# Performance work log

Measured on AMD Instinct MI355X. Metric: run time of the kernel, lower is better.

Reference implementation:

```python
import jax, jax.numpy as jnp
import numpy as np

DIM = 384
HEADS = 12
HD = DIM // HEADS  # 32
WIN = 16
N = WIN * WIN      # 256
B = 256            # num_windows * batch
K = 5              # dwc kernel size
EPS = 1e-6


def setup_inputs() -> dict:
    key = jax.random.key(0)
    ks = jax.random.split(key, 8)
    u = lambda k, shape, fan_in: jax.random.uniform(
        k, shape, jnp.float32, -1.0 / np.sqrt(fan_in), 1.0 / np.sqrt(fan_in))
    return {
        "x": jax.random.normal(ks[0], (B, N, DIM), jnp.float32),
        # nn.Linear(dim, 3*dim): weight [3C, C], bias [3C]
        "qkv_w": u(ks[1], (3 * DIM, DIM), DIM),
        "qkv_b": u(ks[2], (3 * DIM,), DIM),
        # nn.Parameter initialized to zeros
        "pos_enc": jnp.zeros((1, N, DIM), jnp.float32),
        # depthwise Conv2d(HD, HD, K, groups=HD): weight [HD, 1, K, K]
        "dwc_w": u(ks[3], (HD, 1, K, K), K * K),
        "dwc_b": u(ks[4], (HD,), K * K),
        "proj_w": u(ks[5], (DIM, DIM), DIM),
        "proj_b": u(ks[6], (DIM,), DIM),
    }


def reference(x, qkv_w, qkv_b, pos_enc, dwc_w, dwc_b, proj_w, proj_b):
    Bsz, Nn, C = x.shape
    qkv = x @ qkv_w.T + qkv_b                     # [B, N, 3C]
    q, k, v = jnp.split(qkv, 3, axis=-1)          # each [B, N, C]
    k = k + pos_enc
    q = jax.nn.relu(q)
    k = jax.nn.relu(k)

    def to_heads(t):  # 'b n (h c) -> (b h) n c'
        return t.reshape(Bsz, Nn, HEADS, HD).transpose(0, 2, 1, 3).reshape(Bsz * HEADS, Nn, HD)

    q, k, v = to_heads(q), to_heads(k), to_heads(v)
    # explicit fp32 (autocast disabled block in original)
    qf = q.astype(jnp.float32)
    kf = k.astype(jnp.float32)
    vf = v.astype(jnp.float32)

    z = 1.0 / (jnp.einsum('bic,bc->bi', qf, kf.sum(axis=1)) + EPS)  # [BH, N]

    i = j = Nn
    c = d = HD
    if i * j * (c + d) > c * d * (i + j):  # kv-first (true for N=256, HD=32)
        kv = jnp.einsum('bjc,bjd->bcd', kf, vf)            # [BH, c, d]
        out = jnp.einsum('bic,bcd,bi->bid', qf, kv, z)     # [BH, N, d]
    else:
        qk = jnp.einsum('bic,bjc->bij', qf, kf)
        out = jnp.einsum('bij,bjd,bi->bid', qk, vf, z)

    # depthwise conv on v: 'b (w h) c -> b c w h'
    num = int(Nn ** 0.5)
    fm = vf.reshape(Bsz * HEADS, num, num, HD).transpose(0, 3, 1, 2)  # NCHW
    fm = jax.lax.conv_general_dilated(
        fm, dwc_w, window_strides=(1, 1),
        padding=[(K // 2, K // 2), (K // 2, K // 2)],
        dimension_numbers=('NCHW', 'OIHW', 'NCHW'),
        feature_group_count=HD)
    fm = fm + dwc_b[None, :, None, None]
    fm = fm.transpose(0, 2, 3, 1).reshape(Bsz * HEADS, Nn, HD)  # 'b c w h -> b (w h) c'

    out = out + fm
    # '(b h) n c -> b n (h c)'
    out = out.reshape(Bsz, HEADS, Nn, HD).transpose(0, 2, 1, 3).reshape(Bsz, Nn, C)
    return out @ proj_w.T + proj_b
```

## Files before the change

### kernel.cpp

```cpp
#include <hip/hip_runtime.h>
#include <stdint.h>
#include <stddef.h>


typedef _Float16 f16;
typedef __attribute__((ext_vector_type(4))) _Float16 f16x4;
typedef __attribute__((ext_vector_type(8))) _Float16 f16x8;
typedef __attribute__((ext_vector_type(4))) float floatx4;

#define DEV __device__ __forceinline__

DEV void async16(const void* g, void* l) {
  __builtin_amdgcn_global_load_lds(
      (const __attribute__((address_space(1))) void*)g,
      (__attribute__((address_space(3))) void*)l,
      16, 0, 0);
}

DEV floatx4 mfma16(f16x8 a, f16x8 b, floatx4 c) {
  return __builtin_amdgcn_mfma_f32_16x16x32_f16(a, b, c, 0, 0, 0);
}

DEV f16x4 cvt4(float4 v) {
  f16x4 h;
  h[0] = (f16)v.x; h[1] = (f16)v.y; h[2] = (f16)v.z; h[3] = (f16)v.w;
  return h;
}

__global__ __launch_bounds__(256) void qkv_kernel(
    const float* __restrict__ A, const float* __restrict__ W,
    const float* __restrict__ bias, const float* __restrict__ pos,
    f16* __restrict__ q_ws, f16* __restrict__ kT_ws, f16* __restrict__ vT_ws) {
  __shared__ __align__(16) f16 Af[128 * 40];
  __shared__ __align__(16) f16 Wf[128 * 40];
  const int tid = threadIdx.x;
  const int lane = tid & 63, wave = tid >> 6;
  const int quad = lane >> 4, lr = lane & 15;
  const int wm = wave >> 1, wn = wave & 1;
  const int bx = blockIdx.x;
  const int ga = bx / 72, rem = bx - ga * 72;
  const int nblk = rem >> 3, gc = rem & 7;
  const int m0 = (ga * 8 + gc) * 128, n0 = nblk * 128;
  const int srow = tid >> 3, sg = tid & 7;

  floatx4 acc[4][4] = {};
  float4 pa[4], pw[4];

#pragma unroll
  for (int rr = 0; rr < 4; ++rr) {
    const int row = rr * 32 + srow;
    pa[rr] = *(const float4*)(A + (size_t)(m0 + row) * 384 + sg * 4);
    pw[rr] = *(const float4*)(W + (size_t)(n0 + row) * 384 + sg * 4);
  }

  for (int kt = 0; kt < 12; ++kt) {
    __syncthreads();
#pragma unroll
    for (int rr = 0; rr < 4; ++rr) {
      const int row = rr * 32 + srow;
      *(f16x4*)(Af + row * 40 + sg * 4) = cvt4(pa[rr]);
      *(f16x4*)(Wf + row * 40 + sg * 4) = cvt4(pw[rr]);
    }
    __syncthreads();
    if (kt < 11) {
      const int k0 = (kt + 1) * 32;
#pragma unroll
      for (int rr = 0; rr < 4; ++rr) {
        const int row = rr * 32 + srow;
        pa[rr] = *(const float4*)(A + (size_t)(m0 + row) * 384 + k0 + sg * 4);
        pw[rr] = *(const float4*)(W + (size_t)(n0 + row) * 384 + k0 + sg * 4);
      }
    }
    f16x8 af[4], wf[4];
#pragma unroll
    for (int mt = 0; mt < 4; ++mt)
      af[mt] = *(const f16x8*)(Af + (wm * 64 + mt * 16 + lr) * 40 + quad * 8);
#pragma unroll
    for (int nt = 0; nt < 4; ++nt)
      wf[nt] = *(const f16x8*)(Wf + (wn * 64 + nt * 16 + lr) * 40 + quad * 8);
#pragma unroll
    for (int mt = 0; mt < 4; ++mt)
#pragma unroll
      for (int nt = 0; nt < 4; ++nt)
        acc[mt][nt] = mfma16(af[mt], wf[nt], acc[mt][nt]);
  }

  float bv[4];
#pragma unroll
  for (int nt = 0; nt < 4; ++nt)
    bv[nt] = bias[n0 + wn * 64 + nt * 16 + lr];

  const int cls = nblk / 3;
  const int cbase = (nblk - cls * 3) * 128;
  if (cls == 0) {
#pragma unroll
    for (int mt = 0; mt < 4; ++mt) {
#pragma unroll
      for (int r = 0; r < 4; ++r) {
        const int m = m0 + wm * 64 + mt * 16 + quad * 4 + r;
        const int bwin = m >> 8, t = m & 255;
#pragma unroll
        for (int nt = 0; nt < 4; ++nt) {
          const int c = cbase + wn * 64 + nt * 16 + lr;
          const int h = c >> 5, hd = c & 31;
          const float val = fmaxf(acc[mt][nt][r] + bv[nt], 0.f);
          q_ws[(size_t)(bwin * 12 + h) * 8192 + t * 32 + hd] = (f16)val;
        }
      }
    }
  } else {
#pragma unroll
    for (int mt = 0; mt < 4; ++mt) {
      const int mb = m0 + wm * 64 + mt * 16 + quad * 4;
      const int bwin = mb >> 8, t0 = mb & 255;
#pragma unroll
      for (int nt = 0; nt < 4; ++nt) {
        const int c = cbase + wn * 64 + nt * 16 + lr;
        const int h = c >> 5, hd = c & 31;
        f16x4 pk;
        if (cls == 1) {
#pragma unroll
          for (int r = 0; r < 4; ++r)
            pk[r] = (f16)fmaxf(acc[mt][nt][r] + bv[nt] + pos[(t0 + r) * 384 + c], 0.f);
          *(f16x4*)(kT_ws + (size_t)(bwin * 12 + h) * 8192 + hd * 256 + t0) = pk;
        } else {
#pragma unroll
          for (int r = 0; r < 4; ++r)
            pk[r] = (f16)(acc[mt][nt][r] + bv[nt]);
          *(f16x4*)(vT_ws + (size_t)(bwin * 12 + h) * 8192 + hd * 256 + t0) = pk;
        }
      }
    }
  }
}

__global__ __launch_bounds__(256) void attn_kernel(
    const f16* __restrict__ q_ws, const f16* __restrict__ kT_ws,
    const f16* __restrict__ vT_ws, const float* __restrict__ dwc_w,
    const float* __restrict__ dwc_b, f16* __restrict__ y_ws) {
  __shared__ __align__(16) char khb[16640];
  __shared__ __align__(16) char vhb[16640];
  __shared__ __align__(16) float pkv[4 * 32 * 36];
  __shared__ float psum[8 * 32];
  __shared__ float ksum[32];
  __shared__ float zbuf[256];
  __shared__ __align__(16) f16 kvT[32 * 40];

  const int tid = threadIdx.x;
  const int lane = tid & 63, wave = tid >> 6;
  const int quad = lane >> 4, lr = lane & 15;
  const int bh = blockIdx.x;
  const size_t base = (size_t)bh * 8192;

#pragma unroll
  for (int t2 = 0; t2 < 4; ++t2) {
    const int is = wave * 4 + t2;
    async16(kT_ws + base + is * 512 + lane * 8, khb + is * 1040);
    async16(vT_ws + base + is * 512 + lane * 8, vhb + is * 1040);
  }
  __syncthreads();

  {
    const int c = tid & 31, seg = tid >> 5;
    const char* kr = khb + (c >> 1) * 1040 + (c & 1) * 512;
    float s = 0.f;
#pragma unroll
    for (int j8 = 0; j8 < 32; j8 += 8) {
      f16x8 a = *(const f16x8*)(kr + (seg * 32 + j8) * 2);
#pragma unroll
      for (int j = 0; j < 8; ++j) s += (float)a[j];
    }
    psum[seg * 32 + c] = s;
  }
  {
    floatx4 kacc[2][2] = {};
#pragma unroll
    for (int ss = 0; ss < 2; ++ss) {
      const int s = wave * 2 + ss;
      f16x8 ka[2], vb[2];
#pragma unroll
      for (int m2 = 0; m2 < 2; ++m2) {
        const int c = m2 * 16 + lr;
        const size_t off =
            (size_t)(c >> 1) * 1040 + (c & 1) * 512 + (s * 32 + quad * 8) * 2;
        ka[m2] = *(const f16x8*)(khb + off);
        vb[m2] = *(const f16x8*)(vhb + off);
      }
#pragma unroll
      for (int m2 = 0; m2 < 2; ++m2)
#pragma unroll
        for (int n2 = 0; n2 < 2; ++n2)
          kacc[m2][n2] = mfma16(ka[m2], vb[n2], kacc[m2][n2]);
    }
#pragma unroll
    for (int m2 = 0; m2 < 2; ++m2)
#pragma unroll
      for (int n2 = 0; n2 < 2; ++n2)
#pragma unroll
        for (int r = 0; r < 4; ++r)
          pkv[(wave * 32 + m2 * 16 + quad * 4 + r) * 36 + n2 * 16 + lr] =
              kacc[m2][n2][r];
  }
  __syncthreads();

  if (tid < 32) {
    float s = 0.f;
#pragma unroll
    for (int seg = 0; seg < 8; ++seg) s += psum[seg * 32 + tid];
    ksum[tid] = s;
  }
  {
    const int c = tid >> 3, d0 = (tid & 7) * 4;
#pragma unroll
    for (int dd = 0; dd < 4; ++dd) {
      const int d = d0 + dd;
      float s = pkv[(0 * 32 + c) * 36 + d] + pkv[(1 * 32 + c) * 36 + d] +
                pkv[(2 * 32 + c) * 36 + d] + pkv[(3 * 32 + c) * 36 + d];
      kvT[d * 40 + c] = (f16)s;
    }
  }
  {
    uint32_t* fmu = (uint32_t*)khb;
    const int cg = tid & 15, xr = tid >> 4, c0 = cg * 2;
    float a0[16], a1[16];
    const float b0v = dwc_b[c0], b1v = dwc_b[c0 + 1];
#pragma unroll
    for (int yy = 0; yy < 16; ++yy) { a0[yy] = b0v; a1[yy] = b1v; }
    const char* v0 = vhb + cg * 1040;
#pragma unroll
    for (int dx = 0; dx < 5; ++dx) {
      const int xx = xr + dx - 2;
      if (xx < 0 || xx > 15) continue;
      float r0[16], r1[16];
      f16x8 h0 = *(const f16x8*)(v0 + xx * 32);
      f16x8 h1 = *(const f16x8*)(v0 + xx * 32 + 16);
      f16x8 h2 = *(const f16x8*)(v0 + 512 + xx * 32);
      f16x8 h3 = *(const f16x8*)(v0 + 512 + xx * 32 + 16);
#pragma unroll
      for (int j = 0; j < 8; ++j) {
        r0[j] = (float)h0[j]; r0[8 + j] = (float)h1[j];
        r1[j] = (float)h2[j]; r1[8 + j] = (float)h3[j];
      }
#pragma unroll
      for (int dy = 0; dy < 5; ++dy) {
        const float w0 = dwc_w[c0 * 25 + dx * 5 + dy];
        const float w1 = dwc_w[(c0 + 1) * 25 + dx * 5 + dy];
#pragma unroll
        for (int yy = 0; yy < 16; ++yy) {
          const int ys = yy + dy - 2;
          if (ys >= 0 && ys < 16) {
            a0[yy] += w0 * r0[ys];
            a1[yy] += w1 * r1[ys];
          }
        }
      }
    }
#pragma unroll
    for (int yy = 0; yy < 16; ++yy) {
      const uint32_t lo = (uint32_t)__builtin_bit_cast(uint16_t, (f16)a0[yy]);
      const uint32_t hi = (uint32_t)__builtin_bit_cast(uint16_t, (f16)a1[yy]);
      fmu[(xr * 16 + yy) * 16 + cg] = lo | (hi << 16);
    }
  }
  __syncthreads();

  {
    const f16* qrow = q_ws + base + (size_t)tid * 32;
    float dot = 0.f;
#pragma unroll
    for (int c8 = 0; c8 < 32; c8 += 8) {
      f16x8 qq = *(const f16x8*)(qrow + c8);
#pragma unroll
      for (int j = 0; j < 8; ++j) dot += (float)qq[j] * ksum[c8 + j];
    }
    zbuf[tid] = 1.f / (dot + 1e-6f);
  }
  {
    floatx4 oacc[4][2] = {};
    f16x8 qa[4], kb[2];
#pragma unroll
    for (int mm = 0; mm < 4; ++mm)
      qa[mm] = *(const f16x8*)(q_ws + base +
                               (size_t)(wave * 64 + mm * 16 + lr) * 32 + quad * 8);
#pragma unroll
    for (int nt = 0; nt < 2; ++nt)
      kb[nt] = *(const f16x8*)(kvT + (nt * 16 + lr) * 40 + quad * 8);
#pragma unroll
    for (int mm = 0; mm < 4; ++mm)
#pragma unroll
      for (int nt = 0; nt < 2; ++nt)
        oacc[mm][nt] = mfma16(qa[mm], kb[nt], oacc[mm][nt]);

    const f16* fmb = (const f16*)khb;
#pragma unroll
    for (int mm = 0; mm < 4; ++mm) {
#pragma unroll
      for (int r = 0; r < 4; ++r) {
        const int i = wave * 64 + mm * 16 + quad * 4 + r;
        const float zi = zbuf[i];
#pragma unroll
        for (int nt = 0; nt < 2; ++nt) {
          const int d = nt * 16 + lr;
          const float val = oacc[mm][nt][r] * zi + (float)fmb[i * 32 + d];
          y_ws[base + (size_t)i * 32 + d] = (f16)val;
        }
      }
    }
  }
}

__global__ __launch_bounds__(256) void proj_kernel(
    const f16* __restrict__ Y, const float* __restrict__ W,
    const float* __restrict__ bias, float* __restrict__ out) {
  __shared__ __align__(16) f16 Af[128 * 32];
  __shared__ __align__(16) f16 Wf[128 * 40];
  const int tid = threadIdx.x;
  const int lane = tid & 63, wave = tid >> 6;
  const int quad = lane >> 4, lr = lane & 15;
  const int wm = wave >> 1, wn = wave & 1;
  const int bx = blockIdx.x;
  const int ga = bx / 24, rem = bx - ga * 24;
  const int nblk = rem >> 3, gc = rem & 7;
  const int m0 = (ga * 8 + gc) * 128, n0 = nblk * 128;
  const int bwin = m0 >> 8, tbase = m0 & 255;
  const int srow = tid >> 3, sg = tid & 7;

  floatx4 acc[4][4] = {};
  float4 pw[4];
#pragma unroll
  for (int rr = 0; rr < 4; ++rr)
    pw[rr] = *(const float4*)(W + (size_t)(n0 + rr * 32 + srow) * 384 + sg * 4);

  for (int kt = 0; kt < 12; ++kt) {
    __syncthreads();
    {
      const size_t hbase = (size_t)(bwin * 12 + kt) * 8192;
#pragma unroll
      for (int t2 = 0; t2 < 2; ++t2) {
        const int ch = wave * 2 + t2;
        const int trow = tbase + ch * 16 + (lane >> 2);
        async16(Y + hbase + (size_t)trow * 32 + (lane & 3) * 8,
                (char*)Af + ch * 1024);
      }
    }
#pragma unroll
    for (int rr = 0; rr < 4; ++rr)
      *(f16x4*)(Wf + (rr * 32 + srow) * 40 + sg * 4) = cvt4(pw[rr]);
    __syncthreads();
    if (kt < 11) {
      const int k0 = (kt + 1) * 32;
#pragma unroll
      for (int rr = 0; rr < 4; ++rr)
        pw[rr] = *(const float4*)(W + (size_t)(n0 + rr * 32 + srow) * 384 +
                                  k0 + sg * 4);
    }
    f16x8 af[4], wf[4];
#pragma unroll
    for (int mt = 0; mt < 4; ++mt)
      af[mt] = *(const f16x8*)(Af + (wm * 64 + mt * 16 + lr) * 32 + quad * 8);
#pragma unroll
    for (int nt = 0; nt < 4; ++nt)
      wf[nt] = *(const f16x8*)(Wf + (wn * 64 + nt * 16 + lr) * 40 + quad * 8);
#pragma unroll
    for (int mt = 0; mt < 4; ++mt)
#pragma unroll
      for (int nt = 0; nt < 4; ++nt)
        acc[mt][nt] = mfma16(af[mt], wf[nt], acc[mt][nt]);
  }

  float bv[4];
#pragma unroll
  for (int nt = 0; nt < 4; ++nt)
    bv[nt] = bias[n0 + wn * 64 + nt * 16 + lr];
#pragma unroll
  for (int mt = 0; mt < 4; ++mt)
#pragma unroll
    for (int r = 0; r < 4; ++r) {
      const int m = m0 + wm * 64 + mt * 16 + quad * 4 + r;
#pragma unroll
      for (int nt = 0; nt < 4; ++nt) {
        const int n = n0 + wn * 64 + nt * 16 + lr;
        out[(size_t)m * 384 + n] = acc[mt][nt][r] + bv[nt];
      }
    }
}

extern "C" void kernel_launch(void* const* d_in, const int* in_sizes, int n_in,
                              void* d_out, int out_size, void* d_ws, size_t ws_size,
                              hipStream_t stream) {
  const float* x = (const float*)d_in[0];
  const float* qkv_w = (const float*)d_in[1];
  const float* qkv_b = (const float*)d_in[2];
  const float* pos = (const float*)d_in[3];
  const float* dwc_w = (const float*)d_in[4];
  const float* dwc_b = (const float*)d_in[5];
  const float* proj_w = (const float*)d_in[6];
  const float* proj_b = (const float*)d_in[7];
  float* out = (float*)d_out;

  const size_t WS_NEEDED = 150994944;
  if (ws_size < WS_NEEDED) return;

  char* ws = (char*)d_ws;
  f16* q_ws = (f16*)(ws);
  f16* kT_ws = (f16*)(ws + 50331648);
  f16* vT_ws = (f16*)(ws + 100663296);

  qkv_kernel<<<4608, 256, 0, stream>>>(x, qkv_w, qkv_b, pos,
                                       q_ws, kT_ws, vT_ws);
  attn_kernel<<<3072, 256, 0, stream>>>(q_ws, kT_ws, vT_ws,
                                        dwc_w, dwc_b, q_ws );
  proj_kernel<<<1536, 256, 0, stream>>>(q_ws, proj_w, proj_b, out);
}
```

Measured before the change: 408.4 us.

## Pre-convert GEMM operands to fp16 and stream tiles via async LDS loads

Adds a standalone fp32-to-fp16 conversion kernel for x, qkv_w and proj_w, storing the results in scratch space (the output buffer and the freed kT workspace region). The QKV and projection GEMMs then load fp16 tiles straight into XOR-swizzled shared memory with global_load_lds, using a K-tile of 64 instead of 32 and no register round trip or in-kernel conversion. This removes the per-tile conversion work and doubles the work per barrier. In exchange it adds an extra full read and write pass over x, and the async loads are no longer prefetched ahead of compute.

```diff
diff --git a/kernel.cpp b/kernel.cpp
--- a/kernel.cpp
+++ b/kernel.cpp
@@ -27,12 +27,21 @@
   return h;
 }
 
+__global__ __launch_bounds__(256) void cvt_kernel(
+    const float* __restrict__ src, f16* __restrict__ dst, int n4) {
+  const int stride = gridDim.x * 256;
+  for (int i = blockIdx.x * 256 + threadIdx.x; i < n4; i += stride) {
+    float4 v = ((const float4*)src)[i];
+    ((f16x4*)dst)[i] = cvt4(v);
+  }
+}
+
 __global__ __launch_bounds__(256) void qkv_kernel(
-    const float* __restrict__ A, const float* __restrict__ W,
+    const f16* __restrict__ A, const f16* __restrict__ W,
     const float* __restrict__ bias, const float* __restrict__ pos,
     f16* __restrict__ q_ws, f16* __restrict__ kT_ws, f16* __restrict__ vT_ws) {
-  __shared__ __align__(16) f16 Af[128 * 40];
-  __shared__ __align__(16) f16 Wf[128 * 40];
+  __shared__ __align__(16) f16 Af[128 * 64];
+  __shared__ __align__(16) f16 Wf[128 * 64];
   const int tid = threadIdx.x;
   const int lane = tid & 63, wave = tid >> 6;
   const int quad = lane >> 4, lr = lane & 15;
@@ -41,48 +50,47 @@
   const int ga = bx / 72, rem = bx - ga * 72;
   const int nblk = rem >> 3, gc = rem & 7;
   const int m0 = (ga * 8 + gc) * 128, n0 = nblk * 128;
-  const int srow = tid >> 3, sg = tid & 7;
+  const int rl = lane >> 3;
+  const int lcol = (lane & 7) ^ rl;
 
   floatx4 acc[4][4] = {};
-  float4 pa[4], pw[4];
-
-#pragma unroll
-  for (int rr = 0; rr < 4; ++rr) {
-    const int row = rr * 32 + srow;
-    pa[rr] = *(const float4*)(A + (size_t)(m0 + row) * 384 + sg * 4);
-    pw[rr] = *(const float4*)(W + (size_t)(n0 + row) * 384 + sg * 4);
-  }
-
-  for (int kt = 0; kt < 12; ++kt) {
+
+  const f16* ap[4];
+  const f16* wp[4];
+#pragma unroll
+  for (int t2 = 0; t2 < 4; ++t2) {
+    const int row = (wave * 4 + t2) * 8 + rl;
+    ap[t2] = A + (size_t)(m0 + row) * 384 + lcol * 8;
+    wp[t2] = W + (size_t)(n0 + row) * 384 + lcol * 8;
+  }
+
+  for (int kt = 0; kt < 6; ++kt) {
     __syncthreads();
 #pragma unroll
-    for (int rr = 0; rr < 4; ++rr) {
-      const int row = rr * 32 + srow;
-      *(f16x4*)(Af + row * 40 + sg * 4) = cvt4(pa[rr]);
-      *(f16x4*)(Wf + row * 40 + sg * 4) = cvt4(pw[rr]);
+    for (int t2 = 0; t2 < 4; ++t2) {
+      const int ch = wave * 4 + t2;
+      async16(ap[t2] + kt * 64, (char*)Af + ch * 1024);
+      async16(wp[t2] + kt * 64, (char*)Wf + ch * 1024);
     }
     __syncthreads();
-    if (kt < 11) {
-      const int k0 = (kt + 1) * 32;
-#pragma unroll
-      for (int rr = 0; rr < 4; ++rr) {
-        const int row = rr * 32 + srow;
-        pa[rr] = *(const float4*)(A + (size_t)(m0 + row) * 384 + k0 + sg * 4);
-        pw[rr] = *(const float4*)(W + (size_t)(n0 + row) * 384 + k0 + sg * 4);
-      }
-    }
-    f16x8 af[4], wf[4];
-#pragma unroll
-    for (int mt = 0; mt < 4; ++mt)
-      af[mt] = *(const f16x8*)(Af + (wm * 64 + mt * 16 + lr) * 40 + quad * 8);
-#pragma unroll
-    for (int nt = 0; nt < 4; ++nt)
-      wf[nt] = *(const f16x8*)(Wf + (wn * 64 + nt * 16 + lr) * 40 + quad * 8);
-#pragma unroll
-    for (int mt = 0; mt < 4; ++mt)
+#pragma unroll
+    for (int s = 0; s < 2; ++s) {
+      const int pc = ((quad + s * 4) ^ (lr & 7)) * 16;
+      f16x8 af[4], wf[4];
+#pragma unroll
+      for (int mt = 0; mt < 4; ++mt)
+        af[mt] = *(const f16x8*)((const char*)Af +
+                                 (wm * 64 + mt * 16 + lr) * 128 + pc);
 #pragma unroll
       for (int nt = 0; nt < 4; ++nt)
-        acc[mt][nt] = mfma16(af[mt], wf[nt], acc[mt][nt]);
+        wf[nt] = *(const f16x8*)((const char*)Wf +
+                                 (wn * 64 + nt * 16 + lr) * 128 + pc);
+#pragma unroll
+      for (int mt = 0; mt < 4; ++mt)
+#pragma unroll
+        for (int nt = 0; nt < 4; ++nt)
+          acc[mt][nt] = mfma16(af[mt], wf[nt], acc[mt][nt]);
+    }
   }
 
   float bv[4];
@@ -310,10 +318,10 @@
 }
 
 __global__ __launch_bounds__(256) void proj_kernel(
-    const f16* __restrict__ Y, const float* __restrict__ W,
+    const f16* __restrict__ Y, const f16* __restrict__ Wh,
     const float* __restrict__ bias, float* __restrict__ out) {
-  __shared__ __align__(16) f16 Af[128 * 32];
-  __shared__ __align__(16) f16 Wf[128 * 40];
+  __shared__ __align__(16) f16 Af[128 * 64];
+  __shared__ __align__(16) f16 Wf[128 * 64];
   const int tid = threadIdx.x;
   const int lane = tid & 63, wave = tid >> 6;
   const int quad = lane >> 4, lr = lane & 15;
@@ -323,49 +331,48 @@
   const int nblk = rem >> 3, gc = rem & 7;
   const int m0 = (ga * 8 + gc) * 128, n0 = nblk * 128;
   const int bwin = m0 >> 8, tbase = m0 & 255;
-  const int srow = tid >> 3, sg = tid & 7;
+  const int rl = lane >> 3;
+  const int lcol = (lane & 7) ^ rl;
 
   floatx4 acc[4][4] = {};
-  float4 pw[4];
-#pragma unroll
-  for (int rr = 0; rr < 4; ++rr)
-    pw[rr] = *(const float4*)(W + (size_t)(n0 + rr * 32 + srow) * 384 + sg * 4);
-
-  for (int kt = 0; kt < 12; ++kt) {
+
+  const f16* ap[4];
+  const f16* wp[4];
+#pragma unroll
+  for (int t2 = 0; t2 < 4; ++t2) {
+    const int rowl = (wave * 4 + t2) * 8 + rl;
+    ap[t2] = Y + (size_t)(bwin * 12 + (lcol >> 2)) * 8192 +
+             (size_t)(tbase + rowl) * 32 + (lcol & 3) * 8;
+    wp[t2] = Wh + (size_t)(n0 + rowl) * 384 + lcol * 8;
+  }
+
+  for (int kt = 0; kt < 6; ++kt) {
     __syncthreads();
-    {
-      const size_t hbase = (size_t)(bwin * 12 + kt) * 8192;
-#pragma unroll
-      for (int t2 = 0; t2 < 2; ++t2) {
-        const int ch = wave * 2 + t2;
-        const int trow = tbase + ch * 16 + (lane >> 2);
-        async16(Y + hbase + (size_t)trow * 32 + (lane & 3) * 8,
-                (char*)Af + ch * 1024);
-      }
-    }
-#pragma unroll
-    for (int rr = 0; rr < 4; ++rr)
-      *(f16x4*)(Wf + (rr * 32 + srow) * 40 + sg * 4) = cvt4(pw[rr]);
+#pragma unroll
+    for (int t2 = 0; t2 < 4; ++t2) {
+      const int ch = wave * 4 + t2;
+      async16(ap[t2] + (size_t)kt * 16384, (char*)Af + ch * 1024);
+      async16(wp[t2] + kt * 64, (char*)Wf + ch * 1024);
+    }
     __syncthreads();
-    if (kt < 11) {
-      const int k0 = (kt + 1) * 32;
-#pragma unroll
-      for (int rr = 0; rr < 4; ++rr)
-        pw[rr] = *(const float4*)(W + (size_t)(n0 + rr * 32 + srow) * 384 +
-                                  k0 + sg * 4);
-    }
-    f16x8 af[4], wf[4];
-#pragma unroll
-    for (int mt = 0; mt < 4; ++mt)
-      af[mt] = *(const f16x8*)(Af + (wm * 64 + mt * 16 + lr) * 32 + quad * 8);
-#pragma unroll
-    for (int nt = 0; nt < 4; ++nt)
-      wf[nt] = *(const f16x8*)(Wf + (wn * 64 + nt * 16 + lr) * 40 + quad * 8);
-#pragma unroll
-    for (int mt = 0; mt < 4; ++mt)
+#pragma unroll
+    for (int s = 0; s < 2; ++s) {
+      const int pc = ((quad + s * 4) ^ (lr & 7)) * 16;
+      f16x8 af[4], wf[4];
+#pragma unroll
+      for (int mt = 0; mt < 4; ++mt)
+        af[mt] = *(const f16x8*)((const char*)Af +
+                                 (wm * 64 + mt * 16 + lr) * 128 + pc);
 #pragma unroll
       for (int nt = 0; nt < 4; ++nt)
-        acc[mt][nt] = mfma16(af[mt], wf[nt], acc[mt][nt]);
+        wf[nt] = *(const f16x8*)((const char*)Wf +
+                                 (wn * 64 + nt * 16 + lr) * 128 + pc);
+#pragma unroll
+      for (int mt = 0; mt < 4; ++mt)
+#pragma unroll
+        for (int nt = 0; nt < 4; ++nt)
+          acc[mt][nt] = mfma16(af[mt], wf[nt], acc[mt][nt]);
+    }
   }
 
   float bv[4];
@@ -406,9 +413,16 @@
   f16* kT_ws = (f16*)(ws + 50331648);
   f16* vT_ws = (f16*)(ws + 100663296);
 
-  qkv_kernel<<<4608, 256, 0, stream>>>(x, qkv_w, qkv_b, pos,
+  f16* xh = (f16*)d_out;
+  f16* qwh = (f16*)((char*)d_out + 50331648);
+  f16* pwh = (f16*)(ws + 50331648);
+
+  cvt_kernel<<<2048, 256, 0, stream>>>(x, xh, 6291456);
+  cvt_kernel<<<432, 256, 0, stream>>>(qkv_w, qwh, 110592);
+  qkv_kernel<<<4608, 256, 0, stream>>>(xh, qwh, qkv_b, pos,
                                        q_ws, kT_ws, vT_ws);
   attn_kernel<<<3072, 256, 0, stream>>>(q_ws, kT_ws, vT_ws,
                                         dwc_w, dwc_b, q_ws );
-  proj_kernel<<<1536, 256, 0, stream>>>(q_ws, proj_w, proj_b, out);
-}
+  cvt_kernel<<<144, 256, 0, stream>>>(proj_w, pwh, 36864);
+  proj_kernel<<<1536, 256, 0, stream>>>(q_ws, pwh, proj_b, out);
+}
```

Result: faster. 367.0 us (-10.1%).
